# Kernel optimization log

Measured on AMD Instinct MI355X. Metric: run time of the kernel, lower is better.

## Reference

```python
import jax, jax.numpy as jnp
import numpy as np

N_NODES = 100000
N_EDGES = 1600000
IN_DIM = 128
HID = 128
OUT_DIM = 64
EPS = 1e-8


def setup_inputs() -> dict:
    key = jax.random.key(0)
    ks = jax.random.split(key, 10)
    x = jax.random.normal(ks[0], (N_NODES, IN_DIM), dtype=jnp.float32)
    edge_index = jax.random.randint(ks[1], (2, N_EDGES), 0, N_NODES, dtype=jnp.int64)
    edge_attr = jax.random.uniform(ks[2], (N_EDGES, 4), dtype=jnp.float32)
    s1 = 1.0 / np.sqrt(IN_DIM)
    s2 = 1.0 / np.sqrt(HID)
    sr = 1.0 / np.sqrt(2 * HID)
    W1 = jax.random.normal(ks[3], (HID, IN_DIM), dtype=jnp.float32) * s1
    b1 = jnp.zeros((HID,), dtype=jnp.float32)
    W2 = jax.random.normal(ks[4], (HID, HID), dtype=jnp.float32) * s2
    b2 = jnp.zeros((HID,), dtype=jnp.float32)
    Wr = jax.random.normal(ks[5], (OUT_DIM, 2 * HID), dtype=jnp.float32) * sr
    br = jnp.zeros((OUT_DIM,), dtype=jnp.float32)
    return {"x": x, "edge_index": edge_index, "edge_attr": edge_attr,
            "W1": W1, "b1": b1, "W2": W2, "b2": b2, "Wr": Wr, "br": br}


def _edge_weight_from_attr_auto(edge_attr):
    # mean over features, min-max normalize, invert, clamp >= 0
    m = edge_attr.mean(axis=-1)                      # [E]
    m_min, m_max = m.min(), m.max()
    m_norm = (m - m_min) / (m_max - m_min + EPS)
    w = jnp.where(m_max - m_min > EPS, 1.0 - m_norm, jnp.ones_like(m))
    return jnp.clip(w, 0.0)


def reference(x, edge_index, edge_attr, W1, b1, W2, b2, Wr, br):
    N = x.shape[0]
    row, col = edge_index[0], edge_index[1]          # source -> target
    ew = _edge_weight_from_attr_auto(edge_attr)      # [E]
    # GCN normalization with self-loops (self-loop weight = 1.0)
    deg = jax.ops.segment_sum(ew, col, num_segments=N) + 1.0   # [N]
    dis = jax.lax.rsqrt(deg)                         # deg >= 1
    norm = dis[row] * ew * dis[col]                  # [E]

    def gcn(h, W, b):
        hW = h @ W.T                                 # [N, d_out]
        agg = jax.ops.segment_sum(norm[:, None] * hW[row], col, num_segments=N)
        # self-loop contribution: dis[i] * 1.0 * dis[i] * hW[i]
        return agg + (dis * dis)[:, None] * hW + b

    # dropout in eval mode -> identity
    h1 = jax.nn.relu(gcn(x, W1, b1))                 # [N, HID]
    h2 = jax.nn.relu(gcn(h1, W2, b2))                # [N, HID]
    hcat = jnp.concatenate([h1, h2], axis=-1)        # [N, 2*HID] (JK concat)
    return hcat @ Wr.T + br                          # residue-level [N, OUT_DIM]
```

## Files before the change

kernel.cpp:

```cpp
#include <hip/hip_runtime.h>

#define NN 100000
#define NE 1600000
#define HID 128
#define ODIM 64
#define NBK 196
#define BSHIFT 9
#define BGRID 512
#define CHUNK 3125
#define BITER 13
#define BINCAP 12288

typedef unsigned int u32;
typedef unsigned short u16;
typedef __bf16 bf16x8 __attribute__((ext_vector_type(8)));
typedef float f32x4 __attribute__((ext_vector_type(4)));

__device__ __forceinline__ float bf_lo(u32 p){ return __uint_as_float(p << 16); }
__device__ __forceinline__ float bf_hi(u32 p){ return __uint_as_float(p & 0xffff0000u); }
__device__ __forceinline__ u16 f2bf(float f){
  u32 u = __float_as_uint(f);
  u += 0x7fffu + ((u >> 16) & 1u);
  return (u16)(u >> 16);
}
__device__ __forceinline__ bf16x8 ld8bf(const u16* p){ return *(const bf16x8*)p; }
__device__ __forceinline__ bf16x8 cvt8(const float* p){
  union { bf16x8 v; u16 s[8]; } r;
#pragma unroll
  for (int i = 0; i < 8; i++) r.s[i] = f2bf(p[i]);
  return r.v;
}

__global__ __launch_bounds__(256) void k_prep(
    const float* __restrict__ W1, const float* __restrict__ W2,
    const float* __restrict__ Wr, u16* __restrict__ W1b, u16* __restrict__ W2b,
    u16* __restrict__ Wrb, u32* __restrict__ bcur, u32* __restrict__ minmax){
  int i = blockIdx.x * 256 + threadIdx.x;
  const float* src; u16* dst; int off;
  if (i < 4096){ src = W1; dst = W1b; off = i; }
  else if (i < 8192){ src = W2; dst = W2b; off = i - 4096; }
  else { src = Wr; dst = Wrb; off = i - 8192; }
  float4 v = ((const float4*)src)[off];
  uint2 o;
  o.x = (u32)f2bf(v.x) | ((u32)f2bf(v.y) << 16);
  o.y = (u32)f2bf(v.z) | ((u32)f2bf(v.w) << 16);
  ((uint2*)dst)[off] = o;
  if (blockIdx.x == 0){
    if (threadIdx.x < NBK) bcur[threadIdx.x] = (u32)threadIdx.x * BINCAP;
    if (threadIdx.x == 0){ minmax[0] = 0x7f800000u; minmax[1] = 0u; }
  }
}

__global__ __launch_bounds__(256) void k_bin(
    const float* __restrict__ eattr, const int* __restrict__ erow,
    const int* __restrict__ ecol, u32* __restrict__ bcur,
    uint2* __restrict__ bin, u32* __restrict__ minmax){
  __shared__ u32 lcnt[NBK];
  __shared__ u32 gb[NBK];
  int tid = threadIdx.x;
  for (int t = tid; t < NBK; t += 256) lcnt[t] = 0;
  __syncthreads();
  int base = blockIdx.x * CHUNK;
  float lmin = __uint_as_float(0x7f800000u), lmax = 0.f;
  u32 pk[BITER]; float mv[BITER]; u32 sv[BITER];
#pragma unroll
  for (int it = 0; it < BITER; it++){
    int idx = it * 256 + tid;
    u32 p = 0xFFFFFFFFu; float m = 0.f; u32 s = 0;
    if (idx < CHUNK){
      int e = base + idx;
      float4 a = ((const float4*)eattr)[e];
      m = 0.25f * (a.x + a.y + a.z + a.w);
      lmin = fminf(lmin, m); lmax = fmaxf(lmax, m);
      int c = ecol[e];
      s = (u32)erow[e]; if (s >= NN) s = 0;
      if ((u32)c < NN){
        u32 b = (u32)c >> BSHIFT;
        u32 r = atomicAdd(&lcnt[b], 1u);
        p = (b << 21) | (((u32)c & 511u) << 12) | r;
      }
    }
    pk[it] = p; mv[it] = m; sv[it] = s;
  }
  __syncthreads();
  for (int t = tid; t < NBK; t += 256){
    u32 n = lcnt[t];
    u32 na = (n + 7u) & ~7u;
    u32 g = 0x80000000u;
    if (na){
      g = atomicAdd(&bcur[t], na);
      if (g + na <= (u32)(t + 1) * BINCAP){
        uint2 sent; sent.x = 0xFFFFFFFFu; sent.y = 0u;
        for (u32 k = n; k < na; k++) bin[g + k] = sent;
      } else g = 0x80000000u;
    }
    gb[t] = g;
  }
  __syncthreads();
#pragma unroll
  for (int it = 0; it < BITER; it++){
    u32 p = pk[it];
    if (p == 0xFFFFFFFFu) continue;
    u32 g = gb[p >> 21];
    if (g == 0x80000000u) continue;
    uint2 rec; rec.x = sv[it] | (((p >> 12) & 511u) << 17); rec.y = __float_as_uint(mv[it]);
    bin[g + (p & 4095u)] = rec;
  }
  for (int off = 32; off; off >>= 1){
    lmin = fminf(lmin, __shfl_xor(lmin, off));
    lmax = fmaxf(lmax, __shfl_xor(lmax, off));
  }
  __shared__ float smin[4], smax[4];
  int wid = tid >> 6, lane = tid & 63;
  if (lane == 0){ smin[wid] = lmin; smax[wid] = lmax; }
  __syncthreads();
  if (tid == 0){
    float mn = fminf(fminf(smin[0], smin[1]), fminf(smin[2], smin[3]));
    float mx = fmaxf(fmaxf(smax[0], smax[1]), fmaxf(smax[2], smax[3]));
    atomicMin(&minmax[0], __float_as_uint(mn));
    atomicMax(&minmax[1], __float_as_uint(mx));
  }
}

__global__ __launch_bounds__(1024) void k_sort(
    const u32* __restrict__ bcur, const uint2* __restrict__ bin,
    const u32* __restrict__ minmax, int2* __restrict__ csr,
    int* __restrict__ row_start, int* __restrict__ counts, float* __restrict__ dis){
  int b = blockIdx.x;
  int bb = b * BINCAP, be = (int)bcur[b];
  float mn  = __uint_as_float(minmax[0]);
  float mx  = __uint_as_float(minmax[1]);
  float rng = mx - mn;
  bool flat = !(rng > 1e-8f);
  float inv = 1.f / (rng + 1e-8f);
  __shared__ u32 cnt[512], off[512], cur[512], degfx[512];
  int tid = threadIdx.x;
  if (tid < 512){ cnt[tid] = 0; degfx[tid] = 0; }
  __syncthreads();
  for (int i = bb + tid; i < be; i += 1024){
    uint2 r = bin[i];
    if (r.x == 0xFFFFFFFFu) continue;
    u32 d = (r.x >> 17) & 511u;
    float w = flat ? 1.f : fmaxf(1.f - (__uint_as_float(r.y) - mn) * inv, 0.f);
    atomicAdd(&cnt[d], 1u);
    atomicAdd(&degfx[d], (u32)(w * 1048576.f + 0.5f));
  }
  __syncthreads();
  u32 v = 0;
  if (tid < 512){ v = cnt[tid]; off[tid] = v; }
  __syncthreads();
  for (int s = 1; s < 512; s <<= 1){
    u32 t = 0;
    if (tid < 512 && tid >= s) t = off[tid - s];
    __syncthreads();
    if (tid < 512) off[tid] += t;
    __syncthreads();
  }
  if (tid < 512){
    u32 ex = off[tid] - v;
    cur[tid] = ex;
    int node = (b << BSHIFT) + tid;
    if (node < NN){
      row_start[node] = bb + (int)ex;
      counts[node] = (int)v;
      dis[node] = rsqrtf(1.f + (float)degfx[tid] * (1.f / 1048576.f));
    }
  }
  __syncthreads();
  for (int i = bb + tid; i < be; i += 1024){
    uint2 r = bin[i];
    if (r.x == 0xFFFFFFFFu) continue;
    u32 d = (r.x >> 17) & 511u;
    float w = flat ? 1.f : fmaxf(1.f - (__uint_as_float(r.y) - mn) * inv, 0.f);
    u32 pos = (u32)bb + atomicAdd(&cur[d], 1u);
    int2 rec; rec.x = (int)(r.x & 0x1FFFFu); rec.y = __float_as_int(w);
    csr[pos] = rec;
  }
}

template <bool A_F32>
__global__ __launch_bounds__(256) void k_gemm128(
    const void* __restrict__ Av, const u16* __restrict__ Bt,
    const float* __restrict__ dis, u16* __restrict__ G){
  int wave = threadIdx.x >> 6, lane = threadIdx.x & 63;
  int m0 = blockIdx.x * 16;
  int m = lane & 15, q = lane >> 4;
  const float* arow_f = (const float*)Av + (size_t)(m0 + m) * HID;
  const u16*   arow_b = (const u16*)Av   + (size_t)(m0 + m) * HID;
  const u16* brow0 = Bt + (size_t)(wave * 16 + m) * HID;
  const u16* brow1 = brow0 + (size_t)64 * HID;
  f32x4 acc0 = {0.f, 0.f, 0.f, 0.f}, acc1 = {0.f, 0.f, 0.f, 0.f};
#pragma unroll
  for (int kb = 0; kb < HID; kb += 32){
    bf16x8 af = A_F32 ? cvt8(arow_f + kb + q * 8) : ld8bf(arow_b + kb + q * 8);
    acc0 = __builtin_amdgcn_mfma_f32_16x16x32_bf16(af, ld8bf(brow0 + kb + q * 8), acc0, 0, 0, 0);
    acc1 = __builtin_amdgcn_mfma_f32_16x16x32_bf16(af, ld8bf(brow1 + kb + q * 8), acc1, 0, 0, 0);
  }
  u16* crow = G + (size_t)(m0 + q * 4) * HID + wave * 16 + m;
#pragma unroll
  for (int r = 0; r < 4; r++){
    float d = dis[m0 + q * 4 + r];
    crow[(size_t)r * HID]      = f2bf(acc0[r] * d);
    crow[(size_t)r * HID + 64] = f2bf(acc1[r] * d);
  }
}

__global__ __launch_bounds__(256) void k_aggregate(
    const int* __restrict__ row_start, const int* __restrict__ counts,
    const int2* __restrict__ csr, const float* __restrict__ dis,
    const u16* __restrict__ g, const float* __restrict__ bias,
    u16* __restrict__ hout){
  int node = blockIdx.x * 4 + (threadIdx.x >> 6);
  int lane = threadIdx.x & 63;
  int s = row_start[node], c = counts[node];
  const u32* gp = (const u32*)g;
  u32 sv = gp[((size_t)node << 6) + lane];
  float acc0 = bf_lo(sv), acc1 = bf_hi(sv);
  for (int base = 0; base < c; base += 64){
    int nch = min(64, c - base);
    int2 pw; pw.x = 0; pw.y = 0;
    if (lane < nch) pw = csr[s + base + lane];
    int j = 0;
#define GATH(T) \
    for (; j + T <= nch; j += T){ \
      u32 pv[T]; float wv[T]; \
      _Pragma("unroll") \
      for (int t = 0; t < T; t++){ \
        u32 st = (u32)__builtin_amdgcn_readlane(pw.x, j + t); \
        wv[t] = __uint_as_float(__builtin_amdgcn_readlane(pw.y, j + t)); \
        const u32* rowp = gp + st * 64u;          \
        pv[t] = rowp[lane]; \
      } \
      _Pragma("unroll") \
      for (int t = 0; t < T; t++){ \
        acc0 += wv[t] * bf_lo(pv[t]); \
        acc1 += wv[t] * bf_hi(pv[t]); \
      } \
    }
    GATH(16)
    GATH(8)
    GATH(4)
#undef GATH
    for (; j < nch; ++j){
      u32 si = (u32)__builtin_amdgcn_readlane(pw.x, j);
      float wi = __uint_as_float(__builtin_amdgcn_readlane(pw.y, j));
      const u32* rowp = gp + si * 64u;
      u32 pv = rowp[lane];
      acc0 += wi * bf_lo(pv); acc1 += wi * bf_hi(pv);
    }
  }
  float di = dis[node];
  float2 bv = ((const float2*)bias)[lane];
  float o0 = fmaxf(acc0 * di + bv.x, 0.f);
  float o1 = fmaxf(acc1 * di + bv.y, 0.f);
  ((u32*)hout)[((size_t)node << 6) + lane] = (u32)f2bf(o0) | ((u32)f2bf(o1) << 16);
}

__global__ __launch_bounds__(256) void k_readout(
    const u16* __restrict__ h1, const u16* __restrict__ h2,
    const u16* __restrict__ Wrb, const float* __restrict__ br, float* __restrict__ out){
  int wave = threadIdx.x >> 6, lane = threadIdx.x & 63;
  int m0 = blockIdx.x * 16;
  int n0 = wave * 16;
  int m = lane & 15, q = lane >> 4;
  const u16* a1 = h1 + (size_t)(m0 + m) * HID;
  const u16* a2 = h2 + (size_t)(m0 + m) * HID;
  const u16* b  = Wrb + (size_t)(n0 + m) * (2 * HID);
  f32x4 acc = {0.f, 0.f, 0.f, 0.f};
#pragma unroll
  for (int kb = 0; kb < HID; kb += 32){
    acc = __builtin_amdgcn_mfma_f32_16x16x32_bf16(
        ld8bf(a1 + kb + q * 8), ld8bf(b + kb + q * 8), acc, 0, 0, 0);
  }
#pragma unroll
  for (int kb = 0; kb < HID; kb += 32){
    acc = __builtin_amdgcn_mfma_f32_16x16x32_bf16(
        ld8bf(a2 + kb + q * 8), ld8bf(b + HID + kb + q * 8), acc, 0, 0, 0);
  }
  float bias = br[n0 + m];
  float* crow = out + (size_t)(m0 + q * 4) * ODIM + n0 + m;
#pragma unroll
  for (int r = 0; r < 4; r++) crow[(size_t)r * ODIM] = acc[r] + bias;
}

extern "C" void kernel_launch(void* const* d_in, const int* in_sizes, int n_in,
                              void* d_out, int out_size, void* d_ws, size_t ws_size,
                              hipStream_t stream){
  const float* x     = (const float*)d_in[0];
  const int*   eidx  = (const int*)d_in[1];
  const float* eattr = (const float*)d_in[2];
  const float* W1    = (const float*)d_in[3];
  const float* b1    = (const float*)d_in[4];
  const float* W2    = (const float*)d_in[5];
  const float* b2    = (const float*)d_in[6];
  const float* Wr    = (const float*)d_in[7];
  const float* br    = (const float*)d_in[8];
  const int* erow  = eidx;
  const int* ecol  = eidx + NE;

  char* w = (char*)d_ws;
  auto carve = [&](size_t bytes) -> void* {
    void* p = (void*)w;
    w += (bytes + 255) & ~(size_t)255;
    return p;
  };
  int2* csr      = (int2*)carve((size_t)NBK * BINCAP * 8);
  u32* bcur      = (u32*)carve(256 * 4);
  u32* minmax    = (u32*)carve(256);
  int* row_start = (int*)carve((size_t)NN * 4);
  int* counts    = (int*)carve((size_t)NN * 4);
  float* dis     = (float*)carve((size_t)NN * 4);
  u16* W1b       = (u16*)carve((size_t)HID * HID * 2);
  u16* W2b       = (u16*)carve((size_t)HID * HID * 2);
  u16* Wrb       = (u16*)carve((size_t)ODIM * 2 * HID * 2);
  u16* g         = (u16*)carve((size_t)NN * HID * 2);
  u16* h1        = (u16*)carve((size_t)NN * HID * 2);
  u16* h2        = (u16*)carve((size_t)NN * HID * 2);
  uint2* bin     = (uint2*)h2;

  k_prep<<<48, 256, 0, stream>>>(W1, W2, Wr, W1b, W2b, Wrb, bcur, minmax);
  k_bin<<<BGRID, 256, 0, stream>>>(eattr, erow, ecol, bcur, bin, minmax);
  k_sort<<<NBK, 1024, 0, stream>>>(bcur, bin, minmax, csr, row_start, counts, dis);

  k_gemm128<true><<<NN / 16, 256, 0, stream>>>(x, W1b, dis, g);
  k_aggregate<<<NN / 4, 256, 0, stream>>>(row_start, counts, csr, dis, g, b1, h1);
  k_gemm128<false><<<NN / 16, 256, 0, stream>>>(h1, W2b, dis, g);
  k_aggregate<<<NN / 4, 256, 0, stream>>>(row_start, counts, csr, dis, g, b2, h2);
  k_readout<<<NN / 16, 256, 0, stream>>>(h1, h2, Wrb, br, (float*)d_out);
}
```

Baseline: 425.1 us.

## Stage binned edges in LDS, pack CSR into 32-bit, use packed FMA

The binning kernel now computes a block-local prefix scan over bucket counts and stages records in shared memory, then writes them to global bins in contiguous, coalesced runs instead of scattered stores. The CSR record shrinks from 8 bytes to 4 bytes by packing a 17-bit source index with a 15-bit quantized edge weight, which halves CSR traffic in the sort and both aggregation passes. Aggregation accumulates into a float2 vector so the compiler can emit packed FMAs. Quantizing weights to 15 bits adds a small numerical error, and the larger LDS footprint in the binning kernel may lower its occupancy.

```diff
diff --git a/kernel.cpp b/kernel.cpp
--- a/kernel.cpp
+++ b/kernel.cpp
@@ -10,11 +10,14 @@
 #define CHUNK 3125
 #define BITER 13
 #define BINCAP 12288
+#define SMAX 4504
+#define LMAX 568
 
 typedef unsigned int u32;
 typedef unsigned short u16;
 typedef __bf16 bf16x8 __attribute__((ext_vector_type(8)));
 typedef float f32x4 __attribute__((ext_vector_type(4)));
+typedef float f32x2 __attribute__((ext_vector_type(2)));
 
 __device__ __forceinline__ float bf_lo(u32 p){ return __uint_as_float(p << 16); }
 __device__ __forceinline__ float bf_hi(u32 p){ return __uint_as_float(p & 0xffff0000u); }
@@ -55,10 +58,16 @@
     const float* __restrict__ eattr, const int* __restrict__ erow,
     const int* __restrict__ ecol, u32* __restrict__ bcur,
     uint2* __restrict__ bin, u32* __restrict__ minmax){
-  __shared__ u32 lcnt[NBK];
-  __shared__ u32 gb[NBK];
+  __shared__ u32 lcnt[NBK], lofs[NBK], gb[NBK];
+  __shared__ u32 scn[256];
+  __shared__ u16 lmap[LMAX];
+  __shared__ uint2 stage[SMAX];
+  __shared__ u32 Tt;
+  __shared__ float smin[4], smax[4];
   int tid = threadIdx.x;
   for (int t = tid; t < NBK; t += 256) lcnt[t] = 0;
+  uint2 sent; sent.x = 0xFFFFFFFFu; sent.y = 0u;
+  for (int t = tid; t < SMAX; t += 256) stage[t] = sent;
   __syncthreads();
   int base = blockIdx.x * CHUNK;
   float lmin = __uint_as_float(0x7f800000u), lmax = 0.f;
@@ -83,34 +92,46 @@
     pk[it] = p; mv[it] = m; sv[it] = s;
   }
   __syncthreads();
-  for (int t = tid; t < NBK; t += 256){
-    u32 n = lcnt[t];
-    u32 na = (n + 7u) & ~7u;
+  u32 na = 0;
+  if (tid < NBK) na = (lcnt[tid] + 7u) & ~7u;
+  scn[tid] = na; __syncthreads();
+  for (int s = 1; s < 256; s <<= 1){
+    u32 t = (tid >= s) ? scn[tid - s] : 0;
+    __syncthreads();
+    scn[tid] += t;
+    __syncthreads();
+  }
+  u32 ex = scn[tid] - na;
+  if (tid < NBK){
+    lofs[tid] = ex;
     u32 g = 0x80000000u;
     if (na){
-      g = atomicAdd(&bcur[t], na);
-      if (g + na <= (u32)(t + 1) * BINCAP){
-        uint2 sent; sent.x = 0xFFFFFFFFu; sent.y = 0u;
-        for (u32 k = n; k < na; k++) bin[g + k] = sent;
-      } else g = 0x80000000u;
-    }
-    gb[t] = g;
-  }
+      g = atomicAdd(&bcur[tid], na);
+      if (g + na > (u32)(tid + 1) * BINCAP) g = 0x80000000u;
+    }
+    gb[tid] = g;
+    for (u32 l = ex >> 3; l < (ex + na) >> 3; l++) lmap[l] = (u16)tid;
+  }
+  if (tid == 255) Tt = scn[255];
   __syncthreads();
 #pragma unroll
   for (int it = 0; it < BITER; it++){
     u32 p = pk[it];
     if (p == 0xFFFFFFFFu) continue;
-    u32 g = gb[p >> 21];
-    if (g == 0x80000000u) continue;
     uint2 rec; rec.x = sv[it] | (((p >> 12) & 511u) << 17); rec.y = __float_as_uint(mv[it]);
-    bin[g + (p & 4095u)] = rec;
+    stage[lofs[p >> 21] + (p & 4095u)] = rec;
+  }
+  __syncthreads();
+  u32 T = Tt;
+  for (u32 i = tid; i < T; i += 256){
+    u32 b = lmap[i >> 3];
+    u32 g = gb[b];
+    if (g != 0x80000000u) bin[g + (i - lofs[b])] = stage[i];
   }
   for (int off = 32; off; off >>= 1){
     lmin = fminf(lmin, __shfl_xor(lmin, off));
     lmax = fmaxf(lmax, __shfl_xor(lmax, off));
   }
-  __shared__ float smin[4], smax[4];
   int wid = tid >> 6, lane = tid & 63;
   if (lane == 0){ smin[wid] = lmin; smax[wid] = lmax; }
   __syncthreads();
@@ -124,7 +145,7 @@
 
 __global__ __launch_bounds__(1024) void k_sort(
     const u32* __restrict__ bcur, const uint2* __restrict__ bin,
-    const u32* __restrict__ minmax, int2* __restrict__ csr,
+    const u32* __restrict__ minmax, u32* __restrict__ csr,
     int* __restrict__ row_start, int* __restrict__ counts, float* __restrict__ dis){
   int b = blockIdx.x;
   int bb = b * BINCAP, be = (int)bcur[b];
@@ -172,9 +193,9 @@
     if (r.x == 0xFFFFFFFFu) continue;
     u32 d = (r.x >> 17) & 511u;
     float w = flat ? 1.f : fmaxf(1.f - (__uint_as_float(r.y) - mn) * inv, 0.f);
+    u32 wq = (u32)(w * 32767.f + 0.5f);
     u32 pos = (u32)bb + atomicAdd(&cur[d], 1u);
-    int2 rec; rec.x = (int)(r.x & 0x1FFFFu); rec.y = __float_as_int(w);
-    csr[pos] = rec;
+    csr[pos] = (r.x & 0x1FFFFu) | (wq << 17);
   }
 }
 
@@ -207,7 +228,7 @@
 
 __global__ __launch_bounds__(256) void k_aggregate(
     const int* __restrict__ row_start, const int* __restrict__ counts,
-    const int2* __restrict__ csr, const float* __restrict__ dis,
+    const u32* __restrict__ csr, const float* __restrict__ dis,
     const u16* __restrict__ g, const float* __restrict__ bias,
     u16* __restrict__ hout){
   int node = blockIdx.x * 4 + (threadIdx.x >> 6);
@@ -215,26 +236,31 @@
   int s = row_start[node], c = counts[node];
   const u32* gp = (const u32*)g;
   u32 sv = gp[((size_t)node << 6) + lane];
-  float acc0 = bf_lo(sv), acc1 = bf_hi(sv);
+  f32x2 acc = {bf_lo(sv), bf_hi(sv)};
   for (int base = 0; base < c; base += 64){
     int nch = min(64, c - base);
-    int2 pw; pw.x = 0; pw.y = 0;
-    if (lane < nch) pw = csr[s + base + lane];
+    u32 sidx = 0; float ws = 0.f;
+    if (lane < nch){
+      u32 pw = csr[s + base + lane];
+      sidx = pw & 0x1FFFFu;
+      ws = (float)(pw >> 17) * (1.f / 32767.f);
+    }
+    u32 wsb = __float_as_uint(ws);
     int j = 0;
 #define GATH(T) \
     for (; j + T <= nch; j += T){ \
       u32 pv[T]; float wv[T]; \
       _Pragma("unroll") \
       for (int t = 0; t < T; t++){ \
-        u32 st = (u32)__builtin_amdgcn_readlane(pw.x, j + t); \
-        wv[t] = __uint_as_float(__builtin_amdgcn_readlane(pw.y, j + t)); \
+        u32 st = (u32)__builtin_amdgcn_readlane(sidx, j + t); \
+        wv[t] = __uint_as_float(__builtin_amdgcn_readlane(wsb, j + t)); \
         const u32* rowp = gp + st * 64u;          \
         pv[t] = rowp[lane]; \
       } \
       _Pragma("unroll") \
       for (int t = 0; t < T; t++){ \
-        acc0 += wv[t] * bf_lo(pv[t]); \
-        acc1 += wv[t] * bf_hi(pv[t]); \
+        f32x2 val = {bf_lo(pv[t]), bf_hi(pv[t])}; \
+        acc += wv[t] * val; \
       } \
     }
     GATH(16)
@@ -242,17 +268,18 @@
     GATH(4)
 #undef GATH
     for (; j < nch; ++j){
-      u32 si = (u32)__builtin_amdgcn_readlane(pw.x, j);
-      float wi = __uint_as_float(__builtin_amdgcn_readlane(pw.y, j));
-      const u32* rowp = gp + si * 64u;
+      u32 st = (u32)__builtin_amdgcn_readlane(sidx, j);
+      float wt = __uint_as_float(__builtin_amdgcn_readlane(wsb, j));
+      const u32* rowp = gp + st * 64u;
       u32 pv = rowp[lane];
-      acc0 += wi * bf_lo(pv); acc1 += wi * bf_hi(pv);
+      f32x2 val = {bf_lo(pv), bf_hi(pv)};
+      acc += wt * val;
     }
   }
   float di = dis[node];
   float2 bv = ((const float2*)bias)[lane];
-  float o0 = fmaxf(acc0 * di + bv.x, 0.f);
-  float o1 = fmaxf(acc1 * di + bv.y, 0.f);
+  float o0 = fmaxf(acc.x * di + bv.x, 0.f);
+  float o1 = fmaxf(acc.y * di + bv.y, 0.f);
   ((u32*)hout)[((size_t)node << 6) + lane] = (u32)f2bf(o0) | ((u32)f2bf(o1) << 16);
 }
 
@@ -304,7 +331,7 @@
     w += (bytes + 255) & ~(size_t)255;
     return p;
   };
-  int2* csr      = (int2*)carve((size_t)NBK * BINCAP * 8);
+  u32* csr       = (u32*)carve((size_t)NBK * BINCAP * 4);
   u32* bcur      = (u32*)carve(256 * 4);
   u32* minmax    = (u32*)carve(256);
   int* row_start = (int*)carve((size_t)NN * 4);
```

Result: no change. 418.2 us (-1.6%).
